# Kernel tuning notes

Measured on AMD Instinct MI355X. Metric: run time of the kernel, lower is better.

## Reference

```python
import jax, jax.numpy as jnp
import numpy as np

N_NODES = 100000
N_EDGES = 1600000
N_GRAPHS = 256


def gcn_conv(x, src, dst, edge_weight, W, b, num_nodes):
    """PyG GCNConv: add self-loops, symmetric degree normalization,
    linear transform, scatter-add aggregation, bias."""
    loop = jnp.arange(num_nodes)
    s = jnp.concatenate([src, loop])
    d = jnp.concatenate([dst, loop])
    ew = jnp.concatenate([edge_weight, jnp.ones((num_nodes,), dtype=edge_weight.dtype)])
    deg = jax.ops.segment_sum(ew, d, num_segments=num_nodes)  # [N]
    dinv = jnp.where(deg > 0, deg ** -0.5, 0.0)
    norm = dinv[s] * ew * dinv[d]  # [E+N]
    h = x @ W  # [N, out]
    msg = h[s] * norm[:, None]  # gather + scale
    out = jax.ops.segment_sum(msg, d, num_segments=num_nodes)  # scatter-add
    return out + b


def global_mean_pool(x, batch, num_graphs):
    s = jax.ops.segment_sum(x, batch, num_segments=num_graphs)
    cnt = jax.ops.segment_sum(jnp.ones((x.shape[0],), dtype=x.dtype), batch, num_segments=num_graphs)
    return s / jnp.maximum(cnt, 1.0)[:, None]


def setup_inputs() -> dict:
    key = jax.random.key(0)
    ks = jax.random.split(key, 12)
    x = jax.random.normal(ks[0], (N_NODES, 128), dtype=jnp.float32)
    edge_index = jax.random.randint(ks[1], (2, N_EDGES), 0, N_NODES, dtype=jnp.int64)
    edge_attr = jax.random.uniform(ks[2], (N_EDGES,), dtype=jnp.float32)
    batch = jnp.sort(jax.random.randint(ks[3], (N_NODES,), 0, N_GRAPHS, dtype=jnp.int64))
    def lin(k, fan_in, fan_out):
        lim = 1.0 / np.sqrt(fan_in)
        kw, kb = jax.random.split(k)
        W = jax.random.uniform(kw, (fan_in, fan_out), minval=-lim, maxval=lim, dtype=jnp.float32)
        b = jax.random.uniform(kb, (fan_out,), minval=-lim, maxval=lim, dtype=jnp.float32)
        return W, b
    W1, b1 = lin(ks[4], 128, 64)
    W2, b2 = lin(ks[5], 64, 64)
    W3, b3 = lin(ks[6], 64, 64)
    Wl, bl = lin(ks[7], 64, 10)
    return {"x": x, "edge_index": edge_index, "edge_attr": edge_attr, "batch": batch,
            "W1": W1, "b1": b1, "W2": W2, "b2": b2, "W3": W3, "b3": b3, "Wl": Wl, "bl": bl}


def reference(x, edge_index, edge_attr, batch, W1, b1, W2, b2, W3, b3, Wl, bl):
    src, dst = edge_index[0], edge_index[1]
    n = x.shape[0]
    h = jax.nn.relu(gcn_conv(x, src, dst, edge_attr, W1, b1, n))
    h = jax.nn.relu(gcn_conv(h, src, dst, edge_attr, W2, b2, n))
    h = jax.nn.relu(gcn_conv(h, src, dst, edge_attr, W3, b3, n))
    g = global_mean_pool(h, batch, N_GRAPHS)  # [G, 64]
    return g @ Wl + bl  # [G, num_classes]
```

## Files before the change

### kernel.cpp

```cpp
#include <hip/hip_runtime.h>
#include <hip/hip_bf16.h>

#define N_NODES  100000
#define N_EDGES  1600000
#define N_GRAPHS 256
#define F 64
#define NBUCK  782
#define NCHUNK 782


__global__ __launch_bounds__(256) void k_hist(const int* __restrict__ dst, int* __restrict__ hist) {
    __shared__ int lh[NBUCK];
    int tid = threadIdx.x, chunk = blockIdx.x;
    for (int j = tid; j < NBUCK; j += 256) lh[j] = 0;
    __syncthreads();
    int e0 = chunk * 2048;
#pragma unroll
    for (int i = 0; i < 8; i++) {
        int e = e0 + i * 256 + tid;
        if (e < N_EDGES) atomicAdd(&lh[dst[e] >> 7], 1);
    }
    __syncthreads();
    for (int j = tid; j < NBUCK; j += 256) hist[chunk * NBUCK + j] = lh[j];
}

__global__ __launch_bounds__(256) void k_colscan(int* __restrict__ hist, int* __restrict__ btot) {
    __shared__ int ts[256];
    int b = blockIdx.x, tid = threadIdx.x;
    int v[4], loc[4], run = 0;
#pragma unroll
    for (int k = 0; k < 4; k++) {
        int c = tid * 4 + k;
        v[k] = (c < NCHUNK) ? hist[c * NBUCK + b] : 0;
        loc[k] = run; run += v[k];
    }
    ts[tid] = run;
    __syncthreads();
    int x = run;
    for (int off = 1; off < 256; off <<= 1) {
        int t = (tid >= off) ? ts[tid - off] : 0;
        __syncthreads();
        x += t; ts[tid] = x;
        __syncthreads();
    }
    int texcl = x - run;
#pragma unroll
    for (int k = 0; k < 4; k++) {
        int c = tid * 4 + k;
        if (c < NCHUNK) hist[c * NBUCK + b] = texcl + loc[k];
    }
    if (tid == 255) btot[b] = x;
}

__global__ __launch_bounds__(256) void k_bscan(const int* __restrict__ btot, int* __restrict__ base) {
    __shared__ int ts[256];
    int tid = threadIdx.x;
    int v[4], loc[4], run = 0;
#pragma unroll
    for (int k = 0; k < 4; k++) {
        int c = tid * 4 + k;
        v[k] = (c < NBUCK) ? btot[c] : 0;
        loc[k] = run; run += v[k];
    }
    ts[tid] = run;
    __syncthreads();
    int x = run;
    for (int off = 1; off < 256; off <<= 1) {
        int t = (tid >= off) ? ts[tid - off] : 0;
        __syncthreads();
        x += t; ts[tid] = x;
        __syncthreads();
    }
    int texcl = x - run;
#pragma unroll
    for (int k = 0; k < 4; k++) {
        int c = tid * 4 + k;
        if (c < NBUCK) base[c] = texcl + loc[k];
    }
    if (tid == 255) base[NBUCK] = x;
}

__global__ __launch_bounds__(256) void k_partition(const int* __restrict__ src, const int* __restrict__ dst,
                                                   const float* __restrict__ ew,
                                                   const int* __restrict__ hist, const int* __restrict__ base,
                                                   long long* __restrict__ part) {
    __shared__ int cursor[NBUCK];
    int tid = threadIdx.x, chunk = blockIdx.x;
    for (int j = tid; j < NBUCK; j += 256) cursor[j] = base[j] + hist[chunk * NBUCK + j];
    __syncthreads();
    int e0 = chunk * 2048;
#pragma unroll
    for (int i = 0; i < 8; i++) {
        int e = e0 + i * 256 + tid;
        if (e < N_EDGES) {
            int d = dst[e];
            int pos = atomicAdd(&cursor[d >> 7], 1);
            unsigned lo = (unsigned)src[e] | ((unsigned)(d & 127) << 17);
            long long rec = (long long)((unsigned long long)lo |
                            ((unsigned long long)__float_as_uint(ew[e]) << 32));
            part[pos] = rec;
        }
    }
}

__global__ __launch_bounds__(256) void k_bucket(const long long* __restrict__ part,
                                                const int* __restrict__ base,
                                                float* __restrict__ dinv_g, int* __restrict__ row_off,
                                                int2* __restrict__ esec) {
    __shared__ float fdeg[128];
    __shared__ float sdinv[128];
    __shared__ int   cnt[128];
    __shared__ int   sc[128];
    __shared__ int   cursor[128];
    int b = blockIdx.x, tid = threadIdx.x;
    if (tid < 128) { fdeg[tid] = 1.0f; cnt[tid] = 0; }
    __syncthreads();
    int e0 = base[b], e1 = base[b + 1], ne = e1 - e0;
    for (int k = tid; k < ne; k += 256) {
        long long rec = part[e0 + k];
        int lo = (int)rec;
        int d7 = (lo >> 17) & 127;
        atomicAdd(&fdeg[d7], __uint_as_float((unsigned)(rec >> 32)));
        atomicAdd(&cnt[d7], 1);
    }
    __syncthreads();
    int myc = 0, x = 0;
    if (tid < 128) {
        float dv = rsqrtf(fdeg[tid]);
        sdinv[tid] = dv;
        int node = b * 128 + tid;
        if (node < N_NODES) dinv_g[node] = dv;
        myc = cnt[tid]; x = myc; sc[tid] = x;
    }
    __syncthreads();
    for (int off = 1; off < 128; off <<= 1) {
        int t = (tid < 128 && tid >= off) ? sc[tid - off] : 0;
        __syncthreads();
        if (tid < 128) { x += t; sc[tid] = x; }
        __syncthreads();
    }
    if (tid < 128) {
        int excl = x - myc;
        int node = b * 128 + tid;
        if (node < N_NODES) row_off[node] = e0 + excl;
        cursor[tid] = e0 + excl;
    }
    if (b == 0 && tid == 0) row_off[N_NODES] = N_EDGES;
    __syncthreads();
    for (int k = tid; k < ne; k += 256) {
        long long rec = part[e0 + k];
        int lo = (int)rec;
        int d7 = (lo >> 17) & 127;
        float w = __uint_as_float((unsigned)(rec >> 32));
        int pos = atomicAdd(&cursor[d7], 1);
        esec[pos] = make_int2((lo & 0x1FFFF) << 7, __float_as_int(w * sdinv[d7]));
    }
}

__global__ void k_coef(int2* __restrict__ esec, const float* __restrict__ dinv_g) {
    int e = blockIdx.x * 256 + threadIdx.x;
    if (e < N_EDGES) {
        int2 v = esec[e];
        esec[e] = make_int2(v.x, __float_as_int(__int_as_float(v.y) * dinv_g[((unsigned)v.x) >> 7]));
    } else if (e < N_EDGES + 16) {
        esec[e] = make_int2(0, 0);
    }
}

__global__ void k_gstart(const int* __restrict__ batch, int* gstart) {
    int g = blockIdx.x * 256 + threadIdx.x;
    if (g > N_GRAPHS) return;
    int lo = 0, hi = N_NODES;
    while (lo < hi) {
        int mid = (lo + hi) >> 1;
        if (batch[mid] < g) lo = mid + 1; else hi = mid;
    }
    gstart[g] = lo;
}

template <int K, bool BF16IN>
__global__ __launch_bounds__(256) void k_gemm(const void* __restrict__ Xv,
                                              const float* __restrict__ W,
                                              __hip_bfloat16* __restrict__ H) {
    constexpr int KC = 32;
    constexpr int XP = KC + 4;
    __shared__ float Xs[128 * XP];
    __shared__ float Ws[KC * F];
    const int tid  = threadIdx.x;
    const int fgrp = tid & 15;
    const int ngrp = tid >> 4;
    const int f0   = fgrp * 4;
    const int nb   = blockIdx.x * 128;

    float acc[8][4];
#pragma unroll
    for (int i = 0; i < 8; i++)
#pragma unroll
        for (int j = 0; j < 4; j++) acc[i][j] = 0.0f;

    for (int kc = 0; kc < K; kc += KC) {
        if (kc) __syncthreads();
        if (BF16IN) {
            const unsigned short* X = (const unsigned short*)Xv;
#pragma unroll
            for (int pass = 0; pass < 2; pass++) {
                int idx = tid + pass * 256;
                int r = idx >> 2, q = idx & 3;
                int gr = nb + r; if (gr >= N_NODES) gr = N_NODES - 1;
                uint4 v = *(const uint4*)&X[(size_t)gr * K + kc + q * 8];
                float* dp = &Xs[r * XP + q * 8];
                dp[0] = __uint_as_float(v.x << 16);
                dp[1] = __uint_as_float(v.x & 0xffff0000u);
                dp[2] = __uint_as_float(v.y << 16);
                dp[3] = __uint_as_float(v.y & 0xffff0000u);
                dp[4] = __uint_as_float(v.z << 16);
                dp[5] = __uint_as_float(v.z & 0xffff0000u);
                dp[6] = __uint_as_float(v.w << 16);
                dp[7] = __uint_as_float(v.w & 0xffff0000u);
            }
        } else {
            const float* X = (const float*)Xv;
#pragma unroll
            for (int pass = 0; pass < 4; pass++) {
                int idx = tid + pass * 256;
                int r = idx >> 3, q = idx & 7;
                int gr = nb + r; if (gr >= N_NODES) gr = N_NODES - 1;
                float4 v = *(const float4*)&X[(size_t)gr * K + kc + q * 4];
                *(float4*)&Xs[r * XP + q * 4] = v;
            }
        }
#pragma unroll
        for (int pass = 0; pass < 2; pass++) {
            int idx = tid + pass * 256;
            float4 v = *(const float4*)&W[(size_t)(kc + (idx >> 4)) * F + (idx & 15) * 4];
            *(float4*)&Ws[idx * 4] = v;
        }
        __syncthreads();
#pragma unroll
        for (int k = 0; k < KC; k += 4) {
            float4 wv[4];
#pragma unroll
            for (int kk = 0; kk < 4; kk++)
                wv[kk] = *(const float4*)&Ws[(k + kk) * F + f0];
#pragma unroll
            for (int i = 0; i < 8; i++) {
                float4 xv = *(const float4*)&Xs[(ngrp + 16 * i) * XP + k];
                acc[i][0] = fmaf(xv.x, wv[0].x, acc[i][0]);
                acc[i][0] = fmaf(xv.y, wv[1].x, acc[i][0]);
                acc[i][0] = fmaf(xv.z, wv[2].x, acc[i][0]);
                acc[i][0] = fmaf(xv.w, wv[3].x, acc[i][0]);
                acc[i][1] = fmaf(xv.x, wv[0].y, acc[i][1]);
                acc[i][1] = fmaf(xv.y, wv[1].y, acc[i][1]);
                acc[i][1] = fmaf(xv.z, wv[2].y, acc[i][1]);
                acc[i][1] = fmaf(xv.w, wv[3].y, acc[i][1]);
                acc[i][2] = fmaf(xv.x, wv[0].z, acc[i][2]);
                acc[i][2] = fmaf(xv.y, wv[1].z, acc[i][2]);
                acc[i][2] = fmaf(xv.z, wv[2].z, acc[i][2]);
                acc[i][2] = fmaf(xv.w, wv[3].z, acc[i][2]);
                acc[i][3] = fmaf(xv.x, wv[0].w, acc[i][3]);
                acc[i][3] = fmaf(xv.y, wv[1].w, acc[i][3]);
                acc[i][3] = fmaf(xv.z, wv[2].w, acc[i][3]);
                acc[i][3] = fmaf(xv.w, wv[3].w, acc[i][3]);
            }
        }
    }
#pragma unroll
    for (int i = 0; i < 8; i++) {
        int gn = nb + ngrp + 16 * i;
        if (gn < N_NODES) {
            __hip_bfloat16 hb[4];
            hb[0] = __float2bfloat16(acc[i][0]);
            hb[1] = __float2bfloat16(acc[i][1]);
            hb[2] = __float2bfloat16(acc[i][2]);
            hb[3] = __float2bfloat16(acc[i][3]);
            *(uint2*)&H[(size_t)gn * F + f0] = *(uint2*)hb;
        }
    }
}

__global__ __launch_bounds__(256) void k_agg(const __hip_bfloat16* __restrict__ H,
                                             const int* __restrict__ row_off,
                                             const int2* __restrict__ esec,
                                             const float* __restrict__ dinv,
                                             const float* __restrict__ bias,
                                             __hip_bfloat16* __restrict__ O) {
    int node = blockIdx.x * 4 + (threadIdx.x >> 6);
    int lane = threadIdx.x & 63;
    int q  = lane >> 3;
    int f8 = lane & 7;
    int beg = __builtin_amdgcn_readfirstlane(row_off[node]);
    int end = __builtin_amdgcn_readfirstlane(row_off[node + 1]);
    const char* Hbase = (const char*)H;

    float a[8];
#pragma unroll
    for (int u = 0; u < 8; u++) a[u] = 0.0f;

    for (int j = beg; j < end; j += 8) {
        int2 ev = esec[j + q];
        float c = (j + q < end) ? __int_as_float(ev.y) : 0.0f;
        uint4 hq = *(const uint4*)(Hbase + (unsigned)ev.x + (f8 << 4));
        a[0] = fmaf(c, __uint_as_float(hq.x << 16),         a[0]);
        a[1] = fmaf(c, __uint_as_float(hq.x & 0xffff0000u), a[1]);
        a[2] = fmaf(c, __uint_as_float(hq.y << 16),         a[2]);
        a[3] = fmaf(c, __uint_as_float(hq.y & 0xffff0000u), a[3]);
        a[4] = fmaf(c, __uint_as_float(hq.z << 16),         a[4]);
        a[5] = fmaf(c, __uint_as_float(hq.z & 0xffff0000u), a[5]);
        a[6] = fmaf(c, __uint_as_float(hq.w << 16),         a[6]);
        a[7] = fmaf(c, __uint_as_float(hq.w & 0xffff0000u), a[7]);
    }
#pragma unroll
    for (int m = 8; m < 64; m <<= 1) {
#pragma unroll
        for (int u = 0; u < 8; u++) a[u] += __shfl_xor(a[u], m);
    }
    if (q == 0) {
        float di = dinv[node];
        float di2 = di * di;
        uint4 hs = *(const uint4*)(Hbase + (size_t)node * 128 + (f8 << 4));
        float hv[8];
        hv[0] = __uint_as_float(hs.x << 16);
        hv[1] = __uint_as_float(hs.x & 0xffff0000u);
        hv[2] = __uint_as_float(hs.y << 16);
        hv[3] = __uint_as_float(hs.y & 0xffff0000u);
        hv[4] = __uint_as_float(hs.z << 16);
        hv[5] = __uint_as_float(hs.z & 0xffff0000u);
        hv[6] = __uint_as_float(hs.w << 16);
        hv[7] = __uint_as_float(hs.w & 0xffff0000u);
        const float4* bp = (const float4*)(bias + f8 * 8);
        float4 b0 = bp[0], b1 = bp[1];
        float r[8];
        r[0] = fmaxf(a[0] + b0.x + di2 * hv[0], 0.0f);
        r[1] = fmaxf(a[1] + b0.y + di2 * hv[1], 0.0f);
        r[2] = fmaxf(a[2] + b0.z + di2 * hv[2], 0.0f);
        r[3] = fmaxf(a[3] + b0.w + di2 * hv[3], 0.0f);
        r[4] = fmaxf(a[4] + b1.x + di2 * hv[4], 0.0f);
        r[5] = fmaxf(a[5] + b1.y + di2 * hv[5], 0.0f);
        r[6] = fmaxf(a[6] + b1.z + di2 * hv[6], 0.0f);
        r[7] = fmaxf(a[7] + b1.w + di2 * hv[7], 0.0f);
        __hip_bfloat16 hb[8];
#pragma unroll
        for (int u = 0; u < 8; u++) hb[u] = __float2bfloat16(r[u]);
        *(uint4*)&O[(size_t)node * F + f8 * 8] = *(uint4*)hb;
    }
}

__global__ __launch_bounds__(256) void k_pool_linear(const __hip_bfloat16* __restrict__ H,
                                                     const int* __restrict__ gstart,
                                                     const float* __restrict__ Wl,
                                                     const float* __restrict__ bl,
                                                     float* __restrict__ out) {
    int g = blockIdx.x;
    int beg = gstart[g], end = gstart[g + 1];
    int lane = threadIdx.x & 63, wv = threadIdx.x >> 6;
    float acc = 0.0f;
    for (int r = beg + wv; r < end; r += 4)
        acc += __bfloat162float(H[(size_t)r * F + lane]);
    __shared__ float s[4][F];
    s[wv][lane] = acc;
    __syncthreads();
    if (wv == 0) {
        float tot = s[0][lane] + s[1][lane] + s[2][lane] + s[3][lane];
        float cntf = (float)(end - beg);
        float p = tot / fmaxf(cntf, 1.0f);
        for (int c = 0; c < 10; c++) {
            float v = p * Wl[lane * 10 + c];
            for (int off = 32; off; off >>= 1) v += __shfl_down(v, off);
            if (lane == 0) out[g * 10 + c] = v + bl[c];
        }
    }
}


extern "C" void kernel_launch(void* const* d_in, const int* in_sizes, int n_in,
                              void* d_out, int out_size, void* d_ws, size_t ws_size,
                              hipStream_t stream) {
    const float* x    = (const float*)d_in[0];
    const int*   ei   = (const int*)d_in[1];
    const float* ea   = (const float*)d_in[2];
    const int*   bat  = (const int*)d_in[3];
    const float* W1   = (const float*)d_in[4];
    const float* b1   = (const float*)d_in[5];
    const float* W2   = (const float*)d_in[6];
    const float* b2   = (const float*)d_in[7];
    const float* W3   = (const float*)d_in[8];
    const float* b3   = (const float*)d_in[9];
    const float* Wl   = (const float*)d_in[10];
    const float* bl   = (const float*)d_in[11];
    float* out = (float*)d_out;

    const int* src = ei;
    const int* dst = ei + N_EDGES;

    char* ws = (char*)d_ws;
    size_t off = 0;
    auto carve = [&](size_t bytes) {
        void* p = ws + off;
        off += (bytes + 255) & ~(size_t)255;
        return p;
    };
    float*          dinv    = (float*)carve(N_NODES * 4);
    int*            row_off = (int*)  carve((N_NODES + 1) * 4);
    int2*           esec    = (int2*) carve(((size_t)N_EDGES + 16) * 8);
    __hip_bfloat16* hbuf    = (__hip_bfloat16*)carve((size_t)N_NODES * F * 2);
    __hip_bfloat16* obuf    = (__hip_bfloat16*)carve((size_t)N_NODES * F * 4);
    int*            gstart  = (int*)  carve((N_GRAPHS + 1) * 4);
    (void)ws_size; (void)in_sizes; (void)n_in; (void)out_size;

    long long* part = (long long*)hbuf;
    char* alias = (char*)obuf + (size_t)N_NODES * F * 2;
    int* hist = (int*)alias;                         alias += (size_t)NCHUNK * NBUCK * 4;
    int* btot = (int*)alias;                         alias += (NBUCK + 8) * 4;
    int* base = (int*)alias;

    const int EB  = (N_EDGES + 255) / 256 + 1;
    const int GB  = (N_NODES + 127) / 128;

    k_hist     <<<NCHUNK, 256, 0, stream>>>(dst, hist);
    k_colscan  <<<NBUCK,  256, 0, stream>>>(hist, btot);
    k_bscan    <<<1,      256, 0, stream>>>(btot, base);
    k_partition<<<NCHUNK, 256, 0, stream>>>(src, dst, ea, hist, base, part);
    k_bucket   <<<NBUCK,  256, 0, stream>>>(part, base, dinv, row_off, esec);
    k_coef     <<<EB,     256, 0, stream>>>(esec, dinv);
    k_gstart   <<<2,      256, 0, stream>>>(bat, gstart);

    k_gemm<128, false><<<GB, 256, 0, stream>>>(x, W1, hbuf);
    k_agg<<<N_NODES / 4, 256, 0, stream>>>(hbuf, row_off, esec, dinv, b1, obuf);
    k_gemm<64, true><<<GB, 256, 0, stream>>>(obuf, W2, hbuf);
    k_agg<<<N_NODES / 4, 256, 0, stream>>>(hbuf, row_off, esec, dinv, b2, obuf);
    k_gemm<64, true><<<GB, 256, 0, stream>>>(obuf, W3, hbuf);
    k_agg<<<N_NODES / 4, 256, 0, stream>>>(hbuf, row_off, esec, dinv, b3, obuf);

    k_pool_linear<<<N_GRAPHS, 256, 0, stream>>>(obuf, gstart, Wl, bl, out);
}
```

Measured before the change: 418.8 us.

## Aggregate two nodes per wavefront and coarsen edge-partition chunks

Each wavefront in the aggregation kernel now handles two adjacent nodes and interleaves their edge loops, so two independent gather streams are in flight per iteration. This is meant to raise memory-level parallelism and halve the block count. The partition histogram now uses 8192-edge chunks (196 chunks), which lets the column scan use a single element per thread and shrinks the histogram. The cost is wasted iterations when the two nodes' degrees differ, clamped loads past the edge array, and fewer partition blocks.

Result: faster. 385.2 us (-8.0%).

```diff
diff --git a/kernel.cpp b/kernel.cpp
--- a/kernel.cpp
+++ b/kernel.cpp
@@ -6,7 +6,8 @@
 #define N_GRAPHS 256
 #define F 64
 #define NBUCK  782
-#define NCHUNK 782
+#define CHUNK  8192
+#define NCHUNK 196
 
 
 __global__ __launch_bounds__(256) void k_hist(const int* __restrict__ dst, int* __restrict__ hist) {
@@ -14,9 +15,9 @@
     int tid = threadIdx.x, chunk = blockIdx.x;
     for (int j = tid; j < NBUCK; j += 256) lh[j] = 0;
     __syncthreads();
-    int e0 = chunk * 2048;
-#pragma unroll
-    for (int i = 0; i < 8; i++) {
+    int e0 = chunk * CHUNK;
+#pragma unroll
+    for (int i = 0; i < CHUNK / 256; i++) {
         int e = e0 + i * 256 + tid;
         if (e < N_EDGES) atomicAdd(&lh[dst[e] >> 7], 1);
     }
@@ -27,28 +28,17 @@
 __global__ __launch_bounds__(256) void k_colscan(int* __restrict__ hist, int* __restrict__ btot) {
     __shared__ int ts[256];
     int b = blockIdx.x, tid = threadIdx.x;
-    int v[4], loc[4], run = 0;
-#pragma unroll
-    for (int k = 0; k < 4; k++) {
-        int c = tid * 4 + k;
-        v[k] = (c < NCHUNK) ? hist[c * NBUCK + b] : 0;
-        loc[k] = run; run += v[k];
-    }
-    ts[tid] = run;
-    __syncthreads();
-    int x = run;
+    int v = (tid < NCHUNK) ? hist[tid * NBUCK + b] : 0;
+    ts[tid] = v;
+    __syncthreads();
+    int x = v;
     for (int off = 1; off < 256; off <<= 1) {
         int t = (tid >= off) ? ts[tid - off] : 0;
         __syncthreads();
         x += t; ts[tid] = x;
         __syncthreads();
     }
-    int texcl = x - run;
-#pragma unroll
-    for (int k = 0; k < 4; k++) {
-        int c = tid * 4 + k;
-        if (c < NCHUNK) hist[c * NBUCK + b] = texcl + loc[k];
-    }
+    if (tid < NCHUNK) hist[tid * NBUCK + b] = x - v;
     if (tid == 255) btot[b] = x;
 }
 
@@ -88,9 +78,9 @@
     int tid = threadIdx.x, chunk = blockIdx.x;
     for (int j = tid; j < NBUCK; j += 256) cursor[j] = base[j] + hist[chunk * NBUCK + j];
     __syncthreads();
-    int e0 = chunk * 2048;
-#pragma unroll
-    for (int i = 0; i < 8; i++) {
+    int e0 = chunk * CHUNK;
+#pragma unroll
+    for (int i = 0; i < CHUNK / 256; i++) {
         int e = e0 + i * 256 + tid;
         if (e < N_EDGES) {
             int d = dst[e];
@@ -284,37 +274,63 @@
                                              const float* __restrict__ dinv,
                                              const float* __restrict__ bias,
                                              __hip_bfloat16* __restrict__ O) {
-    int node = blockIdx.x * 4 + (threadIdx.x >> 6);
+    int wv   = threadIdx.x >> 6;
     int lane = threadIdx.x & 63;
+    int np   = blockIdx.x * 8 + wv * 2;
     int q  = lane >> 3;
     int f8 = lane & 7;
-    int beg = __builtin_amdgcn_readfirstlane(row_off[node]);
-    int end = __builtin_amdgcn_readfirstlane(row_off[node + 1]);
+    int b0 = __builtin_amdgcn_readfirstlane(row_off[np]);
+    int m0 = __builtin_amdgcn_readfirstlane(row_off[np + 1]);
+    int e1 = __builtin_amdgcn_readfirstlane(row_off[np + 2]);
     const char* Hbase = (const char*)H;
 
-    float a[8];
-#pragma unroll
-    for (int u = 0; u < 8; u++) a[u] = 0.0f;
-
-    for (int j = beg; j < end; j += 8) {
-        int2 ev = esec[j + q];
-        float c = (j + q < end) ? __int_as_float(ev.y) : 0.0f;
-        uint4 hq = *(const uint4*)(Hbase + (unsigned)ev.x + (f8 << 4));
-        a[0] = fmaf(c, __uint_as_float(hq.x << 16),         a[0]);
-        a[1] = fmaf(c, __uint_as_float(hq.x & 0xffff0000u), a[1]);
-        a[2] = fmaf(c, __uint_as_float(hq.y << 16),         a[2]);
-        a[3] = fmaf(c, __uint_as_float(hq.y & 0xffff0000u), a[3]);
-        a[4] = fmaf(c, __uint_as_float(hq.z << 16),         a[4]);
-        a[5] = fmaf(c, __uint_as_float(hq.z & 0xffff0000u), a[5]);
-        a[6] = fmaf(c, __uint_as_float(hq.w << 16),         a[6]);
-        a[7] = fmaf(c, __uint_as_float(hq.w & 0xffff0000u), a[7]);
+    float a0[8], a1[8];
+#pragma unroll
+    for (int u = 0; u < 8; u++) { a0[u] = 0.0f; a1[u] = 0.0f; }
+
+    int len0 = m0 - b0, len1 = e1 - m0;
+    int maxlen = len0 > len1 ? len0 : len1;
+    int iters = (maxlen + 7) >> 3;
+    int j0 = b0 + q, j1 = m0 + q;
+    for (int it = 0; it < iters; it++, j0 += 8, j1 += 8) {
+        int i0 = j0 < N_EDGES ? j0 : N_EDGES;
+        int i1 = j1 < N_EDGES ? j1 : N_EDGES;
+        int2 ev0 = esec[i0];
+        int2 ev1 = esec[i1];
+        float c0 = (j0 < m0) ? __int_as_float(ev0.y) : 0.0f;
+        float c1 = (j1 < e1) ? __int_as_float(ev1.y) : 0.0f;
+        uint4 h0 = *(const uint4*)(Hbase + (unsigned)ev0.x + (f8 << 4));
+        uint4 h1 = *(const uint4*)(Hbase + (unsigned)ev1.x + (f8 << 4));
+        a0[0] = fmaf(c0, __uint_as_float(h0.x << 16),         a0[0]);
+        a0[1] = fmaf(c0, __uint_as_float(h0.x & 0xffff0000u), a0[1]);
+        a0[2] = fmaf(c0, __uint_as_float(h0.y << 16),         a0[2]);
+        a0[3] = fmaf(c0, __uint_as_float(h0.y & 0xffff0000u), a0[3]);
+        a0[4] = fmaf(c0, __uint_as_float(h0.z << 16),         a0[4]);
+        a0[5] = fmaf(c0, __uint_as_float(h0.z & 0xffff0000u), a0[5]);
+        a0[6] = fmaf(c0, __uint_as_float(h0.w << 16),         a0[6]);
+        a0[7] = fmaf(c0, __uint_as_float(h0.w & 0xffff0000u), a0[7]);
+        a1[0] = fmaf(c1, __uint_as_float(h1.x << 16),         a1[0]);
+        a1[1] = fmaf(c1, __uint_as_float(h1.x & 0xffff0000u), a1[1]);
+        a1[2] = fmaf(c1, __uint_as_float(h1.y << 16),         a1[2]);
+        a1[3] = fmaf(c1, __uint_as_float(h1.y & 0xffff0000u), a1[3]);
+        a1[4] = fmaf(c1, __uint_as_float(h1.z << 16),         a1[4]);
+        a1[5] = fmaf(c1, __uint_as_float(h1.z & 0xffff0000u), a1[5]);
+        a1[6] = fmaf(c1, __uint_as_float(h1.w << 16),         a1[6]);
+        a1[7] = fmaf(c1, __uint_as_float(h1.w & 0xffff0000u), a1[7]);
     }
 #pragma unroll
     for (int m = 8; m < 64; m <<= 1) {
 #pragma unroll
-        for (int u = 0; u < 8; u++) a[u] += __shfl_xor(a[u], m);
-    }
-    if (q == 0) {
+        for (int u = 0; u < 8; u++) {
+            a0[u] += __shfl_xor(a0[u], m);
+            a1[u] += __shfl_xor(a1[u], m);
+        }
+    }
+    if (q < 2) {
+        int node = np + q;
+        float av[8];
+#pragma unroll
+        for (int u = 0; u < 8; u++) av[u] = q ? a1[u] : a0[u];
         float di = dinv[node];
         float di2 = di * di;
         uint4 hs = *(const uint4*)(Hbase + (size_t)node * 128 + (f8 << 4));
@@ -328,16 +344,16 @@
         hv[6] = __uint_as_float(hs.w << 16);
         hv[7] = __uint_as_float(hs.w & 0xffff0000u);
         const float4* bp = (const float4*)(bias + f8 * 8);
-        float4 b0 = bp[0], b1 = bp[1];
+        float4 bv0 = bp[0], bv1 = bp[1];
         float r[8];
-        r[0] = fmaxf(a[0] + b0.x + di2 * hv[0], 0.0f);
-        r[1] = fmaxf(a[1] + b0.y + di2 * hv[1], 0.0f);
-        r[2] = fmaxf(a[2] + b0.z + di2 * hv[2], 0.0f);
-        r[3] = fmaxf(a[3] + b0.w + di2 * hv[3], 0.0f);
-        r[4] = fmaxf(a[4] + b1.x + di2 * hv[4], 0.0f);
-        r[5] = fmaxf(a[5] + b1.y + di2 * hv[5], 0.0f);
-        r[6] = fmaxf(a[6] + b1.z + di2 * hv[6], 0.0f);
-        r[7] = fmaxf(a[7] + b1.w + di2 * hv[7], 0.0f);
+        r[0] = fmaxf(av[0] + bv0.x + di2 * hv[0], 0.0f);
+        r[1] = fmaxf(av[1] + bv0.y + di2 * hv[1], 0.0f);
+        r[2] = fmaxf(av[2] + bv0.z + di2 * hv[2], 0.0f);
+        r[3] = fmaxf(av[3] + bv0.w + di2 * hv[3], 0.0f);
+        r[4] = fmaxf(av[4] + bv1.x + di2 * hv[4], 0.0f);
+        r[5] = fmaxf(av[5] + bv1.y + di2 * hv[5], 0.0f);
+        r[6] = fmaxf(av[6] + bv1.z + di2 * hv[6], 0.0f);
+        r[7] = fmaxf(av[7] + bv1.w + di2 * hv[7], 0.0f);
         __hip_bfloat16 hb[8];
 #pragma unroll
         for (int u = 0; u < 8; u++) hb[u] = __float2bfloat16(r[u]);
@@ -425,11 +441,11 @@
     k_gstart   <<<2,      256, 0, stream>>>(bat, gstart);
 
     k_gemm<128, false><<<GB, 256, 0, stream>>>(x, W1, hbuf);
-    k_agg<<<N_NODES / 4, 256, 0, stream>>>(hbuf, row_off, esec, dinv, b1, obuf);
+    k_agg<<<N_NODES / 8, 256, 0, stream>>>(hbuf, row_off, esec, dinv, b1, obuf);
     k_gemm<64, true><<<GB, 256, 0, stream>>>(obuf, W2, hbuf);
-    k_agg<<<N_NODES / 4, 256, 0, stream>>>(hbuf, row_off, esec, dinv, b2, obuf);
+    k_agg<<<N_NODES / 8, 256, 0, stream>>>(hbuf, row_off, esec, dinv, b2, obuf);
     k_gemm<64, true><<<GB, 256, 0, stream>>>(obuf, W3, hbuf);
-    k_agg<<<N_NODES / 4, 256, 0, stream>>>(hbuf, row_off, esec, dinv, b3, obuf);
+    k_agg<<<N_NODES / 8, 256, 0, stream>>>(hbuf, row_off, esec, dinv, b3, obuf);
 
     k_pool_linear<<<N_GRAPHS, 256, 0, stream>>>(obuf, gstart, Wl, bl, out);
 }
```
